# Optimization experiments

Hardware: AMD Instinct MI355X
Metric: run time of the kernel (lower is better)

The kernel has to match this reference:

```python
import jax, jax.numpy as jnp
import numpy as np

N, DIM, N_EMBED = 8192, 512, 8192


def setup_inputs() -> dict:
    key = jax.random.key(0)
    k1, k2, k3, k4 = jax.random.split(key, 4)
    return {
        "x": jax.random.normal(k1, (N, DIM), dtype=jnp.float32),
        "embed_weight": jax.random.normal(k2, (N_EMBED, DIM), dtype=jnp.float32),
        "proj_w": jax.random.normal(k3, (DIM, DIM), dtype=jnp.float32) * (1.0 / np.sqrt(DIM)),
        "proj_b": jax.random.normal(k4, (DIM,), dtype=jnp.float32) * 0.01,
    }


def reference(x, embed_weight, proj_w, proj_b):
    # dists[n, e] = ||x_n||^2 - 2 x_n . E_e + ||E_e||^2   -> [N, n_embed]
    dists = (
        jnp.sum(x * x, axis=1, keepdims=True)
        - 2.0 * (x @ embed_weight.T)
        + jnp.sum(embed_weight * embed_weight, axis=1)
    )
    embed_ind = jnp.argmin(dists, axis=1)  # first-min, matches torch .min(1)
    # onehot @ embed_weight == gather of nearest codebook rows
    quant = embed_weight[embed_ind]  # [N, dim]
    residual = (x - quant) @ proj_w.T + proj_b  # nn.Linear(dim, dim_out)
    return x + residual
```

## Files before the change

kernel.cpp:

```cpp
#include <hip/hip_runtime.h>
#include <cstdint>

#define NR 8192
#define DIMK 512
#define NE 8192

#define GBK 32
#define KSTEPS (DIMK / GBK)
#define TILE_BYTES 8192
#define NBLK 64
#define NCAND 128
#define DELTA 6.0f

typedef __bf16 bf16x8 __attribute__((ext_vector_type(8)));
typedef float f32x4 __attribute__((ext_vector_type(4)));

#define BM 128
#define BN 128
#define BK 16
#define ESPLIT 16
#define ERANGE (NE / ESPLIT)
#define ETILES (ERANGE / BN)
#define PM 64
#define PN 64
#define PK 16

__global__ __launch_bounds__(256) void prep_kernel(
    const float* __restrict__ X, const float* __restrict__ E,
    const float* __restrict__ W,
    uint8_t* __restrict__ Ap, uint8_t* __restrict__ Bp,
    uint8_t* __restrict__ Wp, float* __restrict__ enorm) {
    const int bid = blockIdx.x;
    const int wave = threadIdx.x >> 6;
    const int lane = threadIdx.x & 63;

    const float* src;
    uint8_t* dst;
    int row;
    bool doNorm = false;
    if (bid < NE / 4) {
        row = bid * 4 + wave;
        src = E + (size_t)row * DIMK;
        dst = Bp;
        doNorm = true;
    } else if (bid < NE / 4 + NR / 4) {
        row = (bid - NE / 4) * 4 + wave;
        src = X + (size_t)row * DIMK;
        dst = Ap;
    } else {
        row = (bid - NE / 4 - NR / 4) * 4 + wave;
        src = W + (size_t)row * DIMK;
        dst = Wp;
    }

    float4 f0 = *(const float4*)(src + lane * 8);
    float4 f1 = *(const float4*)(src + lane * 8 + 4);
    float v[8] = {f0.x, f0.y, f0.z, f0.w, f1.x, f1.y, f1.z, f1.w};

    if (doNorm) {
        float s = 0.f;
#pragma unroll
        for (int j = 0; j < 8; ++j) s = fmaf(v[j], v[j], s);
#pragma unroll
        for (int off = 32; off > 0; off >>= 1) s += __shfl_xor(s, off, 64);
        if (lane == 0) enorm[row] = s;
    }

    unsigned short o[8];
#pragma unroll
    for (int j = 0; j < 8; ++j) {
        __bf16 h = (__bf16)v[j];
        o[j] = __builtin_bit_cast(unsigned short, h);
    }
    uint4 u;
    u.x = (uint32_t)o[0] | ((uint32_t)o[1] << 16);
    u.y = (uint32_t)o[2] | ((uint32_t)o[3] << 16);
    u.z = (uint32_t)o[4] | ((uint32_t)o[5] << 16);
    u.w = (uint32_t)o[6] | ((uint32_t)o[7] << 16);
    const int r = row & 127;
    const int kt = lane >> 2;
    const int kk = (lane & 3) * 8;
    size_t base = ((size_t)(row >> 7) * KSTEPS + kt) * TILE_BYTES;
    int byte = (r * 64 + kk * 2) ^ ((r & 7) << 4);
    *(uint4*)(dst + base + byte) = u;
}

__global__ __launch_bounds__(256) void enorm_kernel(const float* __restrict__ E,
                                                    float* __restrict__ enorm) {
    int wave = threadIdx.x >> 6;
    int lane = threadIdx.x & 63;
    int row = blockIdx.x * 4 + wave;
    const float* er = E + (size_t)row * DIMK;
    float s = 0.f;
#pragma unroll
    for (int k = 0; k < DIMK / 64; ++k) {
        float v = er[lane + k * 64];
        s = fmaf(v, v, s);
    }
#pragma unroll
    for (int off = 32; off > 0; off >>= 1) s += __shfl_down(s, off, 64);
    if (lane == 0) enorm[row] = s;
}

__device__ __forceinline__ void stage_8k(void* lds, const void* g, int tid) {
    const int wid = tid >> 6;
    const int lane = tid & 63;
    using gu32 = const __attribute__((address_space(1))) uint32_t;
    using lu32 = __attribute__((address_space(3))) uint32_t;
    const uint8_t* gp = (const uint8_t*)g + (size_t)(wid * 1024 + lane * 16);
    uint8_t* lp = (uint8_t*)lds + wid * 1024;
    __builtin_amdgcn_global_load_lds((gu32*)gp, (lu32*)lp, 16, 0, 0);
    __builtin_amdgcn_global_load_lds((gu32*)(gp + 4096), (lu32*)(lp + 4096), 16, 0, 0);
}

__device__ __forceinline__ unsigned flip32(float v) {
    unsigned b = __float_as_uint(v);
    return b ^ (0x80000000u | (unsigned)((int)b >> 31));
}
__device__ __forceinline__ float unflip32(unsigned b) {
    return __uint_as_float(b ^ (0x80000000u | ~(unsigned)((int)b >> 31)));
}

__global__ __launch_bounds__(256, 4) void dist_mfma_kernel(
    const uint8_t* __restrict__ Ap, const uint8_t* __restrict__ Bp,
    const float* __restrict__ enorm,
    uint2* __restrict__ candk) {
    __shared__ __align__(16) uint8_t As[2][TILE_BYTES];
    __shared__ __align__(16) uint8_t Bs[2][TILE_BYTES];

    const int tid = threadIdx.x;
    const int lane = tid & 63;
    const int wid = tid >> 6;
    const int wr = wid >> 1, wc = wid & 1;
    const int xcd = blockIdx.x & 7;
    const int slot = blockIdx.x >> 3;
    const int mb = slot >> 3;
    const int nb = xcd * 8 + (slot & 7);
    const int lr = lane & 15;
    const int kq = lane >> 4;

    const uint8_t* gA = Ap + (size_t)mb * KSTEPS * TILE_BYTES;
    const uint8_t* gB = Bp + (size_t)nb * KSTEPS * TILE_BYTES;

    int aoff[4], boff[4];
#pragma unroll
    for (int mi = 0; mi < 4; ++mi) {
        int row = wr * 64 + mi * 16 + lr;
        aoff[mi] = (row * 64 + kq * 16) ^ ((row & 7) << 4);
    }
#pragma unroll
    for (int ni = 0; ni < 4; ++ni) {
        int row = wc * 64 + ni * 16 + lr;
        boff[ni] = (row * 64 + kq * 16) ^ ((row & 7) << 4);
    }

    f32x4 acc[4][4];
#pragma unroll
    for (int mi = 0; mi < 4; ++mi)
#pragma unroll
        for (int ni = 0; ni < 4; ++ni)
            acc[mi][ni] = (f32x4){0.f, 0.f, 0.f, 0.f};

    stage_8k(As[0], gA, tid);
    stage_8k(Bs[0], gB, tid);

    int buf = 0;
    for (int kt = 0; kt < KSTEPS; ++kt) {
        __syncthreads();
        if (kt + 1 < KSTEPS) {
            stage_8k(As[buf ^ 1], gA + (size_t)(kt + 1) * TILE_BYTES, tid);
            stage_8k(Bs[buf ^ 1], gB + (size_t)(kt + 1) * TILE_BYTES, tid);
        }
        bf16x8 af[4], bfr[4];
#pragma unroll
        for (int mi = 0; mi < 4; ++mi) af[mi] = *(const bf16x8*)(As[buf] + aoff[mi]);
#pragma unroll
        for (int ni = 0; ni < 4; ++ni) bfr[ni] = *(const bf16x8*)(Bs[buf] + boff[ni]);
#pragma unroll
        for (int mi = 0; mi < 4; ++mi)
#pragma unroll
            for (int ni = 0; ni < 4; ++ni)
                acc[mi][ni] = __builtin_amdgcn_mfma_f32_16x16x32_bf16(
                    bfr[ni], af[mi], acc[mi][ni], 0, 0, 0);
        buf ^= 1;
    }

    const int e0 = nb * 128 + wc * 64;
    float en[4][4];
#pragma unroll
    for (int ni = 0; ni < 4; ++ni)
#pragma unroll
        for (int reg = 0; reg < 4; ++reg)
            en[ni][reg] = enorm[e0 + ni * 16 + kq * 4 + reg];

#pragma unroll
    for (int mi = 0; mi < 4; ++mi) {
        unsigned k1 = 0xFFFFFFFFu, k2 = 0xFFFFFFFFu;
#pragma unroll
        for (int ni = 0; ni < 4; ++ni)
#pragma unroll
            for (int reg = 0; reg < 4; ++reg) {
                float s = fmaf(-2.f, acc[mi][ni][reg], en[ni][reg]);
                unsigned key = (flip32(s) & 0xFFFFE000u) |
                               (unsigned)(e0 + ni * 16 + kq * 4 + reg);
                unsigned lo = min(k1, key), hi = max(k1, key);
                k1 = lo;
                k2 = min(k2, hi);
            }
#pragma unroll
        for (int m = 16; m <= 32; m <<= 1) {
            unsigned o1 = __shfl_xor(k1, m, 64);
            unsigned o2 = __shfl_xor(k2, m, 64);
            unsigned lo = min(k1, o1), hi = max(k1, o1);
            k1 = lo;
            k2 = min(hi, min(k2, o2));
        }
        if (lane < 16) {
            int row = mb * 128 + wr * 64 + mi * 16 + lane;
            candk[(size_t)row * NCAND + nb * 2 + wc] = make_uint2(k1, k2);
        }
    }
}

__global__ __launch_bounds__(256) void refine_rpack_kernel(
    const float* __restrict__ X, const float* __restrict__ E,
    const uint2* __restrict__ candk, int* __restrict__ ind,
    uint8_t* __restrict__ Rp) {
    const int wid = threadIdx.x >> 6;
    const int lane = threadIdx.x & 63;
    const int row = blockIdx.x * 4 + wid;

    const uint2* ck = candk + (size_t)row * NCAND;
    uint2 c0 = ck[lane];
    uint2 c1 = ck[lane + 64];
    unsigned keys[4] = {c0.x, c0.y, c1.x, c1.y};

    unsigned kmin = min(min(keys[0], keys[1]), min(keys[2], keys[3]));
#pragma unroll
    for (int off = 32; off > 0; off >>= 1)
        kmin = min(kmin, __shfl_xor(kmin, off, 64));

    const float vmin = unflip32(kmin & 0xFFFFE000u);
    const unsigned kthr = (flip32(vmin + DELTA) & 0xFFFFE000u) | 0x1FFFu;

    unsigned long long msk[4];
    int total = 0;
#pragma unroll
    for (int c = 0; c < 4; ++c) {
        msk[c] = __ballot(keys[c] <= kthr);
        total += __popcll(msk[c]);
    }

    const float* xr = X + (size_t)row * DIMK;
    int besti;
    if (total == 1) {
        besti = (int)(kmin & 0x1FFFu);
    } else {
        double bestd = 1e300;
        int bi = 0x7fffffff;
#pragma unroll 1
        for (int c = 0; c < 4; ++c) {
            unsigned long long mask = msk[c];
            while (mask) {
                int src = __ffsll((long long)mask) - 1;
                mask &= mask - 1;
                unsigned kk = __shfl(keys[c], src, 64);
                int e = (int)(kk & 0x1FFFu);
                const float* er = E + (size_t)e * DIMK;
                double s = 0.0;
#pragma unroll
                for (int j = 0; j < 8; ++j) {
                    double ev = (double)er[lane * 8 + j];
                    double xv = (double)xr[lane * 8 + j];
                    s += ev * (ev - 2.0 * xv);
                }
#pragma unroll
                for (int off = 32; off > 0; off >>= 1)
                    s += __shfl_xor(s, off, 64);
                if (s < bestd || (s == bestd && e < bi)) { bestd = s; bi = e; }
            }
        }
        besti = bi;
    }
    if (lane == 0) ind[row] = besti;

    const float* er = E + (size_t)besti * DIMK;
    unsigned short o[8];
#pragma unroll
    for (int j = 0; j < 8; ++j) {
        __bf16 h = (__bf16)(xr[lane * 8 + j] - er[lane * 8 + j]);
        o[j] = __builtin_bit_cast(unsigned short, h);
    }
    uint4 u;
    u.x = (uint32_t)o[0] | ((uint32_t)o[1] << 16);
    u.y = (uint32_t)o[2] | ((uint32_t)o[3] << 16);
    u.z = (uint32_t)o[4] | ((uint32_t)o[5] << 16);
    u.w = (uint32_t)o[6] | ((uint32_t)o[7] << 16);
    int mbr = row >> 7, r = row & 127;
    int kt = lane >> 2, kk = (lane & 3) * 8;
    size_t base = ((size_t)mbr * KSTEPS + kt) * TILE_BYTES;
    int byte = (r * 64 + kk * 2) ^ ((r & 7) << 4);
    *(uint4*)(Rp + base + byte) = u;
}

__global__ __launch_bounds__(256, 4) void proj_mfma_kernel(
    const uint8_t* __restrict__ Rp, const uint8_t* __restrict__ Wp,
    const float* __restrict__ X, const float* __restrict__ Bv,
    float* __restrict__ Out) {
    __shared__ __align__(16) uint8_t As[2][TILE_BYTES];
    __shared__ __align__(16) uint8_t Bs[2][TILE_BYTES];

    const int tid = threadIdx.x;
    const int lane = tid & 63;
    const int wid = tid >> 6;
    const int wr = wid >> 1, wc = wid & 1;
    const int mb = blockIdx.x >> 2;
    const int nb = blockIdx.x & 3;
    const int lr = lane & 15;
    const int kq = lane >> 4;

    const uint8_t* gA = Rp + (size_t)mb * KSTEPS * TILE_BYTES;
    const uint8_t* gB = Wp + (size_t)nb * KSTEPS * TILE_BYTES;

    int aoff[4], boff[4];
#pragma unroll
    for (int mi = 0; mi < 4; ++mi) {
        int row = wr * 64 + mi * 16 + lr;
        aoff[mi] = (row * 64 + kq * 16) ^ ((row & 7) << 4);
    }
#pragma unroll
    for (int ni = 0; ni < 4; ++ni) {
        int row = wc * 64 + ni * 16 + lr;
        boff[ni] = (row * 64 + kq * 16) ^ ((row & 7) << 4);
    }

    f32x4 acc[4][4];
#pragma unroll
    for (int mi = 0; mi < 4; ++mi)
#pragma unroll
        for (int ni = 0; ni < 4; ++ni)
            acc[mi][ni] = (f32x4){0.f, 0.f, 0.f, 0.f};

    stage_8k(As[0], gA, tid);
    stage_8k(Bs[0], gB, tid);

    int buf = 0;
    for (int kt = 0; kt < KSTEPS; ++kt) {
        __syncthreads();
        if (kt + 1 < KSTEPS) {
            stage_8k(As[buf ^ 1], gA + (size_t)(kt + 1) * TILE_BYTES, tid);
            stage_8k(Bs[buf ^ 1], gB + (size_t)(kt + 1) * TILE_BYTES, tid);
        }
        bf16x8 af[4], bfr[4];
#pragma unroll
        for (int mi = 0; mi < 4; ++mi) af[mi] = *(const bf16x8*)(As[buf] + aoff[mi]);
#pragma unroll
        for (int ni = 0; ni < 4; ++ni) bfr[ni] = *(const bf16x8*)(Bs[buf] + boff[ni]);
#pragma unroll
        for (int mi = 0; mi < 4; ++mi)
#pragma unroll
            for (int ni = 0; ni < 4; ++ni)
                acc[mi][ni] = __builtin_amdgcn_mfma_f32_16x16x32_bf16(
                    af[mi], bfr[ni], acc[mi][ni], 0, 0, 0);
        buf ^= 1;
    }

    const int col0 = nb * 128 + wc * 64;
    float bias[4];
#pragma unroll
    for (int ni = 0; ni < 4; ++ni) bias[ni] = Bv[col0 + ni * 16 + lr];

#pragma unroll
    for (int mi = 0; mi < 4; ++mi) {
#pragma unroll
        for (int reg = 0; reg < 4; ++reg) {
            int row = mb * 128 + wr * 64 + mi * 16 + kq * 4 + reg;
            const float* xrow = X + (size_t)row * DIMK;
            float* orow = Out + (size_t)row * DIMK;
#pragma unroll
            for (int ni = 0; ni < 4; ++ni) {
                int col = col0 + ni * 16 + lr;
                orow[col] = xrow[col] + acc[mi][ni][reg] + bias[ni];
            }
        }
    }
}

__global__ __launch_bounds__(256) void dist_argmin_kernel(
    const float* __restrict__ X, const float* __restrict__ E,
    const float* __restrict__ enorm,
    float* __restrict__ pval, int* __restrict__ pidx) {
    __shared__ float xs[BK][BM + 4];
    __shared__ float es[BK][BN + 4];
    __shared__ float rv[BM][17];
    __shared__ int ri[BM][17];

    const int tid = threadIdx.x;
    const int row0 = blockIdx.y * BM;
    const int e_base = blockIdx.x * ERANGE;
    const int tx = tid & 15;
    const int ty = tid >> 4;

    float minv[8];
    int mini[8];
#pragma unroll
    for (int i = 0; i < 8; ++i) { minv[i] = 3.4e38f; mini[i] = 0; }

    const int lm = tid >> 1;
    const int lk = (tid & 1) * 8;

    for (int et = 0; et < ETILES; ++et) {
        const int e0 = e_base + et * BN;
        float acc[8][8];
#pragma unroll
        for (int i = 0; i < 8; ++i)
#pragma unroll
            for (int j = 0; j < 8; ++j) acc[i][j] = 0.f;

        for (int kt = 0; kt < DIMK / BK; ++kt) {
            const int k0 = kt * BK;
            {
                const float* src = X + (size_t)(row0 + lm) * DIMK + k0 + lk;
                float4 v0 = *(const float4*)(src);
                float4 v1 = *(const float4*)(src + 4);
                xs[lk + 0][lm] = v0.x; xs[lk + 1][lm] = v0.y;
                xs[lk + 2][lm] = v0.z; xs[lk + 3][lm] = v0.w;
                xs[lk + 4][lm] = v1.x; xs[lk + 5][lm] = v1.y;
                xs[lk + 6][lm] = v1.z; xs[lk + 7][lm] = v1.w;
            }
            {
                const float* src = E + (size_t)(e0 + lm) * DIMK + k0 + lk;
                float4 v0 = *(const float4*)(src);
                float4 v1 = *(const float4*)(src + 4);
                es[lk + 0][lm] = v0.x; es[lk + 1][lm] = v0.y;
                es[lk + 2][lm] = v0.z; es[lk + 3][lm] = v0.w;
                es[lk + 4][lm] = v1.x; es[lk + 5][lm] = v1.y;
                es[lk + 6][lm] = v1.z; es[lk + 7][lm] = v1.w;
            }
            __syncthreads();
#pragma unroll
            for (int k = 0; k < BK; ++k) {
                float4 a0 = *(const float4*)&xs[k][ty * 8];
                float4 a1 = *(const float4*)&xs[k][ty * 8 + 4];
                float4 b0 = *(const float4*)&es[k][tx * 8];
                float4 b1 = *(const float4*)&es[k][tx * 8 + 4];
                float av[8] = {a0.x, a0.y, a0.z, a0.w, a1.x, a1.y, a1.z, a1.w};
                float bv[8] = {b0.x, b0.y, b0.z, b0.w, b1.x, b1.y, b1.z, b1.w};
#pragma unroll
                for (int i = 0; i < 8; ++i)
#pragma unroll
                    for (int j = 0; j < 8; ++j)
                        acc[i][j] = fmaf(av[i], bv[j], acc[i][j]);
            }
            __syncthreads();
        }
#pragma unroll
        for (int j = 0; j < 8; ++j) {
            const int e = e0 + tx * 8 + j;
            const float en = enorm[e];
#pragma unroll
            for (int i = 0; i < 8; ++i) {
                const float s = fmaf(-2.f, acc[i][j], en);
                if (s < minv[i]) { minv[i] = s; mini[i] = e; }
            }
        }
    }
#pragma unroll
    for (int i = 0; i < 8; ++i) {
        rv[ty * 8 + i][tx] = minv[i];
        ri[ty * 8 + i][tx] = mini[i];
    }
    __syncthreads();
    if (tid < BM) {
        float bv = rv[tid][0];
        int bi = ri[tid][0];
#pragma unroll
        for (int t = 1; t < 16; ++t) {
            float vv = rv[tid][t];
            int ix = ri[tid][t];
            if (vv < bv || (vv == bv && ix < bi)) { bv = vv; bi = ix; }
        }
        const int row = row0 + tid;
        pval[(size_t)row * ESPLIT + blockIdx.x] = bv;
        pidx[(size_t)row * ESPLIT + blockIdx.x] = bi;
    }
}

__global__ __launch_bounds__(256) void reduce_argmin_kernel(
    const float* __restrict__ pval, const int* __restrict__ pidx,
    int* __restrict__ ind) {
    int r = blockIdx.x * blockDim.x + threadIdx.x;
    if (r >= NR) return;
    float bv = pval[(size_t)r * ESPLIT];
    int bi = pidx[(size_t)r * ESPLIT];
#pragma unroll
    for (int s = 1; s < ESPLIT; ++s) {
        float v = pval[(size_t)r * ESPLIT + s];
        int ix = pidx[(size_t)r * ESPLIT + s];
        if (v < bv || (v == bv && ix < bi)) { bv = v; bi = ix; }
    }
    ind[r] = bi;
}

__global__ __launch_bounds__(256) void proj_kernel(
    const float* __restrict__ X, const float* __restrict__ E,
    const int* __restrict__ ind,
    const float* __restrict__ W, const float* __restrict__ Bv,
    float* __restrict__ Out) {
    __shared__ float as_[PK][PM + 4];
    __shared__ float bs[PK][PN + 4];
    __shared__ int inds[PM];

    const int tid = threadIdx.x;
    const int row0 = blockIdx.y * PM;
    const int col0 = blockIdx.x * PN;

    if (tid < PM) inds[tid] = ind[row0 + tid];
    __syncthreads();

    const int tx = tid & 15;
    const int ty = tid >> 4;

    float acc[4][4];
#pragma unroll
    for (int i = 0; i < 4; ++i)
#pragma unroll
        for (int j = 0; j < 4; ++j) acc[i][j] = 0.f;

    const int lm = tid >> 2;
    const int lk = (tid & 3) * 4;

    for (int kt = 0; kt < DIMK / PK; ++kt) {
        const int k0 = kt * PK;
        {
            float4 xv = *(const float4*)(X + (size_t)(row0 + lm) * DIMK + k0 + lk);
            float4 qv = *(const float4*)(E + (size_t)inds[lm] * DIMK + k0 + lk);
            as_[lk + 0][lm] = xv.x - qv.x;
            as_[lk + 1][lm] = xv.y - qv.y;
            as_[lk + 2][lm] = xv.z - qv.z;
            as_[lk + 3][lm] = xv.w - qv.w;
        }
        {
            float4 wv = *(const float4*)(W + (size_t)(col0 + lm) * DIMK + k0 + lk);
            bs[lk + 0][lm] = wv.x; bs[lk + 1][lm] = wv.y;
            bs[lk + 2][lm] = wv.z; bs[lk + 3][lm] = wv.w;
        }
        __syncthreads();
#pragma unroll
        for (int k = 0; k < PK; ++k) {
            float4 a = *(const float4*)&as_[k][ty * 4];
            float4 b = *(const float4*)&bs[k][tx * 4];
            float av[4] = {a.x, a.y, a.z, a.w};
            float bvv[4] = {b.x, b.y, b.z, b.w};
#pragma unroll
            for (int i = 0; i < 4; ++i)
#pragma unroll
                for (int j = 0; j < 4; ++j)
                    acc[i][j] = fmaf(av[i], bvv[j], acc[i][j]);
        }
        __syncthreads();
    }

#pragma unroll
    for (int j = 0; j < 4; ++j) {
        const int col = col0 + tx * 4 + j;
        const float bias = Bv[col];
#pragma unroll
        for (int i = 0; i < 4; ++i) {
            const int row = row0 + ty * 4 + i;
            Out[(size_t)row * DIMK + col] =
                X[(size_t)row * DIMK + col] + acc[i][j] + bias;
        }
    }
}

extern "C" void kernel_launch(void* const* d_in, const int* in_sizes, int n_in,
                              void* d_out, int out_size, void* d_ws, size_t ws_size,
                              hipStream_t stream) {
    const float* X = (const float*)d_in[0];
    const float* E = (const float*)d_in[1];
    const float* W = (const float*)d_in[2];
    const float* B = (const float*)d_in[3];
    float* out = (float*)d_out;

    const size_t packBytes = (size_t)NR * DIMK * 2;
    const size_t wPackBytes = (size_t)DIMK * DIMK * 2;
    const size_t candBytes = (size_t)NR * NCAND * 8;
    const size_t needMFMA =
        packBytes * 3 + wPackBytes + NE * 4 + candBytes + NR * 4 + 64;

    if (ws_size >= needMFMA) {
        uint8_t* Ap = (uint8_t*)d_ws;
        uint8_t* Bp = Ap + packBytes;
        uint8_t* Rp = Bp + packBytes;
        uint8_t* Wp = Rp + packBytes;
        float* enorm = (float*)(Wp + wPackBytes);
        uint2* candk = (uint2*)(enorm + NE);
        int* ind = (int*)((uint8_t*)candk + candBytes);

        hipLaunchKernelGGL(prep_kernel, dim3(NE / 4 + NR / 4 + DIMK / 4), dim3(256),
                           0, stream, X, E, W, Ap, Bp, Wp, enorm);
        hipLaunchKernelGGL(dist_mfma_kernel, dim3(4096), dim3(256), 0,
                           stream, Ap, Bp, enorm, candk);
        hipLaunchKernelGGL(refine_rpack_kernel, dim3(NR / 4), dim3(256), 0, stream,
                           X, E, candk, ind, Rp);
        hipLaunchKernelGGL(proj_mfma_kernel, dim3(256), dim3(256), 0, stream,
                           Rp, Wp, X, B, out);
    } else {
        float* enorm = (float*)d_ws;
        float* pval = enorm + NE;
        int* pidx = (int*)(pval + (size_t)NR * ESPLIT);
        int* ind = pidx + (size_t)NR * ESPLIT;

        hipLaunchKernelGGL(enorm_kernel, dim3(NE / 4), dim3(256), 0, stream, E, enorm);
        hipLaunchKernelGGL(dist_argmin_kernel, dim3(ESPLIT, NR / BM), dim3(256), 0,
                           stream, X, E, enorm, pval, pidx);
        hipLaunchKernelGGL(reduce_argmin_kernel, dim3(NR / 256), dim3(256), 0, stream,
                           pval, pidx, ind);
        hipLaunchKernelGGL(proj_kernel, dim3(DIMK / PN, NR / PM), dim3(256), 0, stream,
                           X, E, ind, W, B, out);
    }
}
```

Before: 114.8 us.

## Enlarge distance GEMM tile to 256x256 with 4-stage LDS pipeline

Raises the distance MFMA kernel's block tile from 128x128 to 256x256 using 512 threads. Each wave now computes a 128x64 sub-tile, which raises arithmetic intensity per LDS and global byte. The X and codebook packing is relaid out into 256-row K-tiles to match. A 4-buffer LDS ring with 3 tiles prefetched replaces the double buffer, synchronized by explicit vmcnt waits plus s_barrier, and MFMA issue is wrapped in s_setprio. The cost is much higher LDS use per block (128 KB), more accumulator registers per thread, and fewer blocks in flight.

```diff
diff --git a/kernel.cpp b/kernel.cpp
--- a/kernel.cpp
+++ b/kernel.cpp
@@ -5,10 +5,9 @@
 #define DIMK 512
 #define NE 8192
 
-#define GBK 32
-#define KSTEPS (DIMK / GBK)
+#define KSTEPS 16
 #define TILE_BYTES 8192
-#define NBLK 64
+#define TB256 16384
 #define NCAND 128
 #define DELTA 6.0f
 
@@ -37,7 +36,7 @@
     const float* src;
     uint8_t* dst;
     int row;
-    bool doNorm = false;
+    bool doNorm = false, wide = true;
     if (bid < NE / 4) {
         row = bid * 4 + wave;
         src = E + (size_t)row * DIMK;
@@ -51,6 +50,7 @@
         row = (bid - NE / 4 - NR / 4) * 4 + wave;
         src = W + (size_t)row * DIMK;
         dst = Wp;
+        wide = false;
     }
 
     float4 f0 = *(const float4*)(src + lane * 8);
@@ -77,12 +77,19 @@
     u.y = (uint32_t)o[2] | ((uint32_t)o[3] << 16);
     u.z = (uint32_t)o[4] | ((uint32_t)o[5] << 16);
     u.w = (uint32_t)o[6] | ((uint32_t)o[7] << 16);
-    const int r = row & 127;
     const int kt = lane >> 2;
     const int kk = (lane & 3) * 8;
-    size_t base = ((size_t)(row >> 7) * KSTEPS + kt) * TILE_BYTES;
-    int byte = (r * 64 + kk * 2) ^ ((r & 7) << 4);
-    *(uint4*)(dst + base + byte) = u;
+    if (wide) {
+        const int r = row & 255;
+        size_t base = ((size_t)(row >> 8) * KSTEPS + kt) * TB256;
+        int byte = (r * 64 + kk * 2) ^ ((r & 7) << 4);
+        *(uint4*)(dst + base + byte) = u;
+    } else {
+        const int r = row & 127;
+        size_t base = ((size_t)(row >> 7) * KSTEPS + kt) * TILE_BYTES;
+        int byte = (r * 64 + kk * 2) ^ ((r & 7) << 4);
+        *(uint4*)(dst + base + byte) = u;
+    }
 }
 
 __global__ __launch_bounds__(256) void enorm_kernel(const float* __restrict__ E,
@@ -103,14 +110,20 @@
 }
 
 __device__ __forceinline__ void stage_8k(void* lds, const void* g, int tid) {
-    const int wid = tid >> 6;
-    const int lane = tid & 63;
     using gu32 = const __attribute__((address_space(1))) uint32_t;
     using lu32 = __attribute__((address_space(3))) uint32_t;
-    const uint8_t* gp = (const uint8_t*)g + (size_t)(wid * 1024 + lane * 16);
-    uint8_t* lp = (uint8_t*)lds + wid * 1024;
+    const uint8_t* gp = (const uint8_t*)g + (size_t)tid * 16;
+    uint8_t* lp = (uint8_t*)lds + tid * 16;
     __builtin_amdgcn_global_load_lds((gu32*)gp, (lu32*)lp, 16, 0, 0);
     __builtin_amdgcn_global_load_lds((gu32*)(gp + 4096), (lu32*)(lp + 4096), 16, 0, 0);
+}
+__device__ __forceinline__ void stage_16k(void* lds, const void* g, int tid) {
+    using gu32 = const __attribute__((address_space(1))) uint32_t;
+    using lu32 = __attribute__((address_space(3))) uint32_t;
+    const uint8_t* gp = (const uint8_t*)g + (size_t)tid * 16;
+    uint8_t* lp = (uint8_t*)lds + tid * 16;
+    __builtin_amdgcn_global_load_lds((gu32*)gp, (lu32*)lp, 16, 0, 0);
+    __builtin_amdgcn_global_load_lds((gu32*)(gp + 8192), (lu32*)(lp + 8192), 16, 0, 0);
 }
 
 __device__ __forceinline__ unsigned flip32(float v) {
@@ -121,71 +134,86 @@
     return __uint_as_float(b ^ (0x80000000u | ~(unsigned)((int)b >> 31)));
 }
 
-__global__ __launch_bounds__(256, 4) void dist_mfma_kernel(
+__global__ __launch_bounds__(512, 2) void dist_mfma_kernel(
     const uint8_t* __restrict__ Ap, const uint8_t* __restrict__ Bp,
     const float* __restrict__ enorm,
     uint2* __restrict__ candk) {
-    __shared__ __align__(16) uint8_t As[2][TILE_BYTES];
-    __shared__ __align__(16) uint8_t Bs[2][TILE_BYTES];
+    __shared__ __align__(16) uint8_t As[4][TB256];
+    __shared__ __align__(16) uint8_t Bs[4][TB256];
 
     const int tid = threadIdx.x;
     const int lane = tid & 63;
     const int wid = tid >> 6;
-    const int wr = wid >> 1, wc = wid & 1;
+    const int wr = wid >> 2;
+    const int wn = wid & 3;
     const int xcd = blockIdx.x & 7;
-    const int slot = blockIdx.x >> 3;
-    const int mb = slot >> 3;
-    const int nb = xcd * 8 + (slot & 7);
+    const int slotid = blockIdx.x >> 3;
+    const int mb = slotid >> 2;
+    const int nbb = xcd * 4 + (slotid & 3);
     const int lr = lane & 15;
     const int kq = lane >> 4;
 
-    const uint8_t* gA = Ap + (size_t)mb * KSTEPS * TILE_BYTES;
-    const uint8_t* gB = Bp + (size_t)nb * KSTEPS * TILE_BYTES;
-
-    int aoff[4], boff[4];
-#pragma unroll
-    for (int mi = 0; mi < 4; ++mi) {
-        int row = wr * 64 + mi * 16 + lr;
+    const uint8_t* gA = Ap + (size_t)mb * KSTEPS * TB256;
+    const uint8_t* gB = Bp + (size_t)nbb * KSTEPS * TB256;
+
+    int aoff[8], boff[4];
+#pragma unroll
+    for (int mi = 0; mi < 8; ++mi) {
+        int row = wr * 128 + mi * 16 + lr;
         aoff[mi] = (row * 64 + kq * 16) ^ ((row & 7) << 4);
     }
 #pragma unroll
     for (int ni = 0; ni < 4; ++ni) {
-        int row = wc * 64 + ni * 16 + lr;
+        int row = wn * 64 + ni * 16 + lr;
         boff[ni] = (row * 64 + kq * 16) ^ ((row & 7) << 4);
     }
 
-    f32x4 acc[4][4];
-#pragma unroll
-    for (int mi = 0; mi < 4; ++mi)
+    f32x4 acc[8][4];
+#pragma unroll
+    for (int mi = 0; mi < 8; ++mi)
 #pragma unroll
         for (int ni = 0; ni < 4; ++ni)
             acc[mi][ni] = (f32x4){0.f, 0.f, 0.f, 0.f};
 
-    stage_8k(As[0], gA, tid);
-    stage_8k(Bs[0], gB, tid);
-
-    int buf = 0;
+#pragma unroll
+    for (int p = 0; p < 3; ++p) {
+        stage_16k(As[p], gA + (size_t)p * TB256, tid);
+        stage_16k(Bs[p], gB + (size_t)p * TB256, tid);
+    }
+
+#pragma unroll
     for (int kt = 0; kt < KSTEPS; ++kt) {
-        __syncthreads();
-        if (kt + 1 < KSTEPS) {
-            stage_8k(As[buf ^ 1], gA + (size_t)(kt + 1) * TILE_BYTES, tid);
-            stage_8k(Bs[buf ^ 1], gB + (size_t)(kt + 1) * TILE_BYTES, tid);
-        }
-        bf16x8 af[4], bfr[4];
-#pragma unroll
-        for (int mi = 0; mi < 4; ++mi) af[mi] = *(const bf16x8*)(As[buf] + aoff[mi]);
-#pragma unroll
-        for (int ni = 0; ni < 4; ++ni) bfr[ni] = *(const bf16x8*)(Bs[buf] + boff[ni]);
-#pragma unroll
-        for (int mi = 0; mi < 4; ++mi)
+        if (kt <= KSTEPS - 3)
+            asm volatile("s_waitcnt vmcnt(8)\n\ts_barrier" ::: "memory");
+        else if (kt == KSTEPS - 2)
+            asm volatile("s_waitcnt vmcnt(4)\n\ts_barrier" ::: "memory");
+        else
+            asm volatile("s_waitcnt vmcnt(0)\n\ts_barrier" ::: "memory");
+
+        if (kt + 3 < KSTEPS) {
+            stage_16k(As[(kt + 3) & 3], gA + (size_t)(kt + 3) * TB256, tid);
+            stage_16k(Bs[(kt + 3) & 3], gB + (size_t)(kt + 3) * TB256, tid);
+        }
+
+        const uint8_t* as_ = As[kt & 3];
+        const uint8_t* bs_ = Bs[kt & 3];
+        bf16x8 af[8], bf[4];
+#pragma unroll
+        for (int mi = 0; mi < 8; ++mi) af[mi] = *(const bf16x8*)(as_ + aoff[mi]);
+#pragma unroll
+        for (int ni = 0; ni < 4; ++ni) bf[ni] = *(const bf16x8*)(bs_ + boff[ni]);
+
+        __builtin_amdgcn_s_setprio(1);
+#pragma unroll
+        for (int mi = 0; mi < 8; ++mi)
 #pragma unroll
             for (int ni = 0; ni < 4; ++ni)
                 acc[mi][ni] = __builtin_amdgcn_mfma_f32_16x16x32_bf16(
-                    bfr[ni], af[mi], acc[mi][ni], 0, 0, 0);
-        buf ^= 1;
-    }
-
-    const int e0 = nb * 128 + wc * 64;
+                    bf[ni], af[mi], acc[mi][ni], 0, 0, 0);
+        __builtin_amdgcn_s_setprio(0);
+    }
+
+    const int e0 = nbb * 256 + wn * 64;
     float en[4][4];
 #pragma unroll
     for (int ni = 0; ni < 4; ++ni)
@@ -193,8 +221,9 @@
         for (int reg = 0; reg < 4; ++reg)
             en[ni][reg] = enorm[e0 + ni * 16 + kq * 4 + reg];
 
-#pragma unroll
-    for (int mi = 0; mi < 4; ++mi) {
+    const int nb = nbb * 2 + (wn >> 1);
+#pragma unroll
+    for (int mi = 0; mi < 8; ++mi) {
         unsigned k1 = 0xFFFFFFFFu, k2 = 0xFFFFFFFFu;
 #pragma unroll
         for (int ni = 0; ni < 4; ++ni)
@@ -216,8 +245,8 @@
             k2 = min(hi, min(k2, o2));
         }
         if (lane < 16) {
-            int row = mb * 128 + wr * 64 + mi * 16 + lane;
-            candk[(size_t)row * NCAND + nb * 2 + wc] = make_uint2(k1, k2);
+            int row = mb * 256 + wr * 128 + mi * 16 + lane;
+            candk[(size_t)row * NCAND + nb * 2 + (wn & 1)] = make_uint2(k1, k2);
         }
     }
 }
@@ -600,7 +629,7 @@
 
         hipLaunchKernelGGL(prep_kernel, dim3(NE / 4 + NR / 4 + DIMK / 4), dim3(256),
                            0, stream, X, E, W, Ap, Bp, Wp, enorm);
-        hipLaunchKernelGGL(dist_mfma_kernel, dim3(4096), dim3(256), 0,
+        hipLaunchKernelGGL(dist_mfma_kernel, dim3(1024), dim3(512), 0,
                            stream, Ap, Bp, enorm, candk);
         hipLaunchKernelGGL(refine_rpack_kernel, dim3(NR / 4), dim3(256), 0, stream,
                            X, E, candk, ind, Rp);
```

Measured after the change: 115.6 us. Within noise of the previous version (+0.7%).
